# Optimization experiments

Hardware: AMD Instinct MI355X
Metric: run time of the kernel (lower is better)

Reference implementation:

```python
import jax, jax.numpy as jnp
import numpy as np

B, T = 64, 20          # batch, caption length
C, HW = 512, 196       # cnn_channels, width*height (14x14)
V, E, U = 10000, 256, 512  # n_tokens, emb_size, lstm_units
MAX_NORM = 5.0


def setup_inputs() -> dict:
    key = jax.random.key(0)
    ks = jax.random.split(key, 12)
    s = 0.02
    return {
        "image_features": jax.random.normal(ks[0], (B, C, HW), jnp.float32),
        "captions_ix": jax.random.randint(ks[1], (B, T), 0, V, dtype=jnp.int32),
        "W_h0": jax.random.normal(ks[2], (U, C), jnp.float32) * s,
        "b_h0": jnp.zeros((U,), jnp.float32),
        "W_c0": jax.random.normal(ks[3], (U, C), jnp.float32) * s,
        "b_c0": jnp.zeros((U,), jnp.float32),
        "emb": jax.random.normal(ks[4], (V, E), jnp.float32) * s,
        "W_key": jax.random.normal(ks[5], (U, C), jnp.float32) * s,
        "b_key": jnp.zeros((U,), jnp.float32),
        "W_ih": jax.random.normal(ks[6], (4 * U, C + E), jnp.float32) * s,
        "b_ih": jnp.zeros((4 * U,), jnp.float32),
        "W_hh": jax.random.normal(ks[7], (4 * U, U), jnp.float32) * s,
        "b_hh": jnp.zeros((4 * U,), jnp.float32),
        "W_out": jax.random.normal(ks[8], (V, C + E + U), jnp.float32) * s,
        "b_out": jnp.zeros((V,), jnp.float32),
    }


def _caption_net(image_features, captions_ix, W_h0, b_h0, W_c0, b_c0, emb,
                 W_key, b_key, W_ih, b_ih, W_hh, b_hh, W_out, b_out):
    feats_mean = image_features.mean(axis=2)                # [B, C]
    hid0 = feats_mean @ W_h0.T + b_h0                       # [B, U]
    cell0 = feats_mean @ W_c0.T + b_c0                      # [B, U]
    feats = jnp.transpose(image_features, (0, 2, 1))        # [B, HW, C]
    keys = feats @ W_key.T + b_key                          # [B, HW, U]

    # nn.Embedding(max_norm=5): renorm rows whose L2 norm exceeds 5
    norms = jnp.linalg.norm(emb, axis=1, keepdims=True)
    emb_eff = emb * jnp.minimum(1.0, MAX_NORM / jnp.maximum(norms, 1e-12))
    cap_emb = emb_eff[captions_ix]                          # [B, T, E]

    inv_scale = 1.0 / (keys.shape[2] ** 0.5)

    def step(carry, emb_t):
        hid, cell = carry
        # scaled dot-product attention, query = current hidden state
        scores = jnp.einsum('bu,bku->bk', hid, keys) * inv_scale   # [B, HW]
        w = jax.nn.softmax(scores, axis=1)
        a = jnp.einsum('bk,bkc->bc', w, feats)                     # [B, C]
        x = jnp.concatenate([emb_t, a], axis=1)                    # [B, E+C]
        gates = x @ W_ih.T + b_ih + hid @ W_hh.T + b_hh            # [B, 4U]
        i, f, g, o = jnp.split(gates, 4, axis=1)
        cell = jax.nn.sigmoid(f) * cell + jax.nn.sigmoid(i) * jnp.tanh(g)
        hid = jax.nn.sigmoid(o) * jnp.tanh(cell)
        out = jnp.concatenate([hid, a, emb_t], axis=1)             # [B, U+C+E]
        return (hid, cell), (out, w)

    (_, _), (outs, attn) = jax.lax.scan(step, (hid0, cell0),
                                        jnp.transpose(cap_emb, (1, 0, 2)))
    outs = jnp.transpose(outs, (1, 0, 2))                   # [B, T, U+C+E]
    attn = jnp.transpose(attn, (1, 0, 2))                   # [B, T, HW]
    logits = outs @ W_out.T + b_out                         # [B, T, V]
    return logits, attn


def reference(image_features, captions_ix, W_h0, b_h0, W_c0, b_c0, emb,
              W_key, b_key, W_ih, b_ih, W_hh, b_hh, W_out, b_out):
    return _caption_net(image_features, captions_ix, W_h0, b_h0, W_c0, b_c0,
                        emb, W_key, b_key, W_ih, b_ih, W_hh, b_hh, W_out, b_out)
```

## Files before the change

kernel.cpp:

```cpp
#include <hip/hip_runtime.h>
#include <math.h>

#define B 64
#define T 20
#define C 512
#define HW 196
#define V 10000
#define E 256
#define U 512
#define G4U 2048
#define ODIM 1280
#define KTOT 1280
#define NBLK 64

typedef short bf8_t __attribute__((ext_vector_type(8)));
typedef float f4_t  __attribute__((ext_vector_type(4)));
typedef _Float16 h2_t __attribute__((ext_vector_type(2)));

__device__ __forceinline__ unsigned short f2bf(float f) {
    unsigned int u = __float_as_uint(f);
    return (unsigned short)((u + 0x7fffu + ((u >> 16) & 1u)) >> 16);
}
__device__ __forceinline__ float bf2f(unsigned short s) {
    return __uint_as_float((unsigned int)s << 16);
}
__device__ __forceinline__ float bflo(unsigned int kv) { return __uint_as_float(kv << 16); }
__device__ __forceinline__ float bfhi(unsigned int kv) { return __uint_as_float(kv & 0xffff0000u); }
__device__ __forceinline__ unsigned short f2h(float f) {
    _Float16 h = (_Float16)f;
    return *(unsigned short*)&h;
}

__device__ __forceinline__ void coh_load4w(const void* p, uint4& r) {
    asm volatile("global_load_dwordx4 %0, %1, off sc0 sc1\n\t"
                 "s_waitcnt vmcnt(0)"
                 : "=&v"(r) : "v"(p) : "memory");
}
__device__ __forceinline__ void coh_load4_issue(const void* p, uint4& r) {
    asm volatile("global_load_dwordx4 %0, %1, off sc0 sc1"
                 : "=&v"(r) : "v"(p) : "memory");
}
__device__ __forceinline__ void wait_vm0() {
    asm volatile("s_waitcnt vmcnt(0)" ::: "memory");
    __builtin_amdgcn_sched_barrier(0);
}
__device__ __forceinline__ void coh_store1f(void* p, float v) {
    asm volatile("global_store_dword %0, %1, off sc0 sc1" :: "v"(p), "v"(v) : "memory");
}
__device__ __forceinline__ void coh_store1u(void* p, unsigned int v) {
    asm volatile("global_store_dword %0, %1, off sc0 sc1" :: "v"(p), "v"(v) : "memory");
}
__device__ __forceinline__ void coh_store_us(void* p, unsigned int v) {
    asm volatile("global_store_short %0, %1, off sc0 sc1" :: "v"(p), "v"(v) : "memory");
}
__device__ __forceinline__ int coh_load_int(const int* p) {
    int v;
    asm volatile("global_load_dword %0, %1, off sc0 sc1\n\t"
                 "s_waitcnt vmcnt(0)"
                 : "=v"(v) : "v"(p) : "memory");
    return v;
}
__device__ __forceinline__ void coh_store_int(int* p, int v) {
    asm volatile("global_store_dword %0, %1, off sc0 sc1" :: "v"(p), "v"(v) : "memory");
}

__device__ __forceinline__ void gbarf(int* barf, int e) {
    asm volatile("s_waitcnt vmcnt(0)" ::: "memory");
    __syncthreads();
    int tid = threadIdx.x;
    if (blockIdx.x == 0) {
        if (tid == 0) coh_store_int(barf + 16, e);
        if (tid < 64) {
            while (!__all(coh_load_int(barf + 16 + tid * 16) >= e)) {}
            if (tid == 0) coh_store_int(barf, e);
        }
    } else {
        if (tid == 0) {
            coh_store_int(barf + 16 + blockIdx.x * 16, e);
            while (coh_load_int(barf) < e) {}
        }
    }
    __syncthreads();
}

__global__ void k_mean(const float* __restrict__ img, float* __restrict__ fm) {
    int wave = threadIdx.x >> 6;
    int lane = threadIdx.x & 63;
    int row = blockIdx.x * 4 + wave;
    const float* p = img + (size_t)row * HW;
    float s = p[lane] + p[lane + 64] + p[lane + 128];
    if (lane < 4) s += p[lane + 192];
    for (int off = 32; off > 0; off >>= 1) s += __shfl_down(s, off, 64);
    if (lane == 0) fm[row] = s * (1.0f / HW);
}

__global__ void k_init(const float* __restrict__ fm,
                       const float* __restrict__ W_h0, const float* __restrict__ b_h0,
                       const float* __restrict__ W_c0, const float* __restrict__ b_c0,
                       unsigned short* __restrict__ xb, float* __restrict__ cell) {
    int wv = blockIdx.x * 4 + (threadIdx.x >> 6);
    int lane = threadIdx.x & 63;
    int which = wv >> 15;
    int r = wv & 32767;
    int b = r >> 9, u = r & 511;
    const float* W = which ? W_c0 : W_h0;
    const float* bias = which ? b_c0 : b_h0;
    const float* f = fm + b * C;
    const float* w = W + (size_t)u * C;
    float s = 0.f;
    #pragma unroll
    for (int c = 0; c < C; c += 64) s += f[c + lane] * w[c + lane];
    for (int off = 32; off > 0; off >>= 1) s += __shfl_down(s, off, 64);
    if (lane == 0) {
        float v = s + bias[u];
        if (which) cell[r] = v;
        else       xb[(size_t)b * KTOT + 768 + u] = f2bf(v);
    }
}

__global__ void k_wkt(const float* __restrict__ Wk, float* __restrict__ WkT) {
    __shared__ float tile[64][65];
    int u0 = blockIdx.x * 64, c0 = blockIdx.y * 64;
    int x = threadIdx.x & 63, y0 = threadIdx.x >> 6;
    #pragma unroll
    for (int i = 0; i < 16; i++) {
        int r = y0 * 16 + i;
        tile[r][x] = Wk[(size_t)(u0 + r) * C + c0 + x];
    }
    __syncthreads();
    #pragma unroll
    for (int i = 0; i < 16; i++) {
        int r = y0 * 16 + i;
        WkT[(size_t)(c0 + r) * U + u0 + x] = tile[x][r];
    }
}

__global__ __launch_bounds__(256) void k_keys(const float* __restrict__ img,
        const float* __restrict__ WkT, const float* __restrict__ b_key,
        unsigned short* __restrict__ keys2) {
    __shared__ unsigned short st[32][200];
    int b = blockIdx.x >> 4;
    int u0 = (blockIdx.x & 15) * 32;
    int wave = __builtin_amdgcn_readfirstlane(threadIdx.x >> 6);
    int lane = threadIdx.x & 63;
    int lk = lane < 49 ? lane : 48;
    const f4_t* imgb = (const f4_t*)(img + (size_t)b * C * HW);
    f4_t acc[8];
    #pragma unroll
    for (int j = 0; j < 8; j++) acc[j] = (f4_t){0.f, 0.f, 0.f, 0.f};
    const float* wp = WkT + u0 + wave * 8;
    for (int c = 0; c < C; c++) {
        f4_t v = imgb[c * 49 + lk];
        const float* w = wp + (size_t)c * U;
        #pragma unroll
        for (int j = 0; j < 8; j++) acc[j] += v * w[j];
    }
    if (lane < 49) {
        #pragma unroll
        for (int j = 0; j < 8; j++) {
            float bk = b_key[u0 + wave * 8 + j];
            int ul = wave * 8 + j;
            int k = lane * 4;
            st[ul][k + 0] = f2bf(acc[j].x + bk);
            st[ul][k + 1] = f2bf(acc[j].y + bk);
            st[ul][k + 2] = f2bf(acc[j].z + bk);
            st[ul][k + 3] = f2bf(acc[j].w + bk);
        }
    }
    __syncthreads();
    int ui = threadIdx.x & 15;
    int kr = threadIdx.x >> 4;
    #pragma unroll
    for (int pass = 0; pass < 13; pass++) {
        int k = pass * 16 + kr;
        if (k < HW) {
            unsigned int lo = st[ui * 2][k];
            unsigned int hi = st[ui * 2 + 1][k];
            *(unsigned int*)&keys2[((size_t)b * HW + k) * U + u0 + ui * 2] = (hi << 16) | lo;
        }
    }
}

__global__ void k_wg(const float* __restrict__ W_ih, const float* __restrict__ W_hh,
                     unsigned short* __restrict__ Wg) {
    int j = blockIdx.x;
    int tid = threadIdx.x;
    const float* s1 = W_ih + (size_t)j * 768;
    const float* s2 = W_hh + (size_t)j * 512;
    unsigned short* dst = Wg + (size_t)j * KTOT;
    #pragma unroll
    for (int p = 0; p < 3; p++) dst[tid + p * 256] = f2bf(s1[tid + p * 256]);
    #pragma unroll
    for (int p = 0; p < 2; p++) dst[768 + tid + p * 256] = f2bf(s2[tid + p * 256]);
}

__global__ void k_emb(const int* __restrict__ ix, const float* __restrict__ emb,
                      unsigned short* __restrict__ outs, int* __restrict__ barf) {
    int bt = blockIdx.x;
    int e = threadIdx.x;
    if (bt == 0) {
        for (int i = e; i < 1040; i += 256) barf[i] = 0;
    }
    int row = ix[bt];
    float v = emb[(size_t)row * E + e];
    __shared__ float red[4];
    float sq = v * v;
    for (int off = 32; off > 0; off >>= 1) sq += __shfl_down(sq, off, 64);
    int wave = e >> 6, lane = e & 63;
    if (lane == 0) red[wave] = sq;
    __syncthreads();
    float norm = sqrtf(red[0] + red[1] + red[2] + red[3]);
    float scale = fminf(1.0f, 5.0f / fmaxf(norm, 1e-12f));
    outs[(size_t)bt * ODIM + (U + C) + e] = f2bf(v * scale);
}

__global__ __launch_bounds__(256) void k_img(const float* __restrict__ img,
                                             unsigned short* __restrict__ img2) {
    int oid = blockIdx.x * 256 + threadIdx.x;
    int row = oid / 25, p = oid - row * 25;
    const float* src = img + (size_t)row * HW;
    unsigned short h[8];
    #pragma unroll
    for (int i = 0; i < 8; i++) {
        int k = p * 8 + i;
        float f = (k < HW) ? src[k] : 0.f;
        h[i] = f2h(f);
    }
    *(uint4*)&img2[(size_t)row * 200 + p * 8] = *(const uint4*)h;
}

__global__ __launch_bounds__(256) void k_wo(const float* __restrict__ W,
                                            unsigned short* __restrict__ Wb) {
    size_t i = ((size_t)blockIdx.x * 256 + threadIdx.x) * 8;
    float4 f0 = *(const float4*)(W + i);
    float4 f1 = *(const float4*)(W + i + 4);
    uint4 q;
    q.x = ((unsigned int)f2bf(f0.y) << 16) | f2bf(f0.x);
    q.y = ((unsigned int)f2bf(f0.w) << 16) | f2bf(f0.z);
    q.z = ((unsigned int)f2bf(f1.y) << 16) | f2bf(f1.x);
    q.w = ((unsigned int)f2bf(f1.w) << 16) | f2bf(f1.z);
    *(uint4*)(Wb + i) = q;
}

__global__ __launch_bounds__(512) void k_loop(
    unsigned short* __restrict__ outs, unsigned short* __restrict__ xb,
    const float* __restrict__ cell0, float* __restrict__ gates4,
    const unsigned short* __restrict__ keys2, const float* __restrict__ img,
    const unsigned short* __restrict__ img2,
    const float* __restrict__ b_ih, const float* __restrict__ b_hh,
    const unsigned short* __restrict__ Wg, float* __restrict__ attn,
    int* __restrict__ barf) {
    int b = blockIdx.x;
    int tid = threadIdx.x;
    int wave = __builtin_amdgcn_readfirstlane(tid >> 6);
    int lane = tid & 63;
    int m16 = lane & 15, quad = lane >> 4;
    __shared__ float hidS[U];
    __shared__ float wS[200];
    __shared__ float red[8];
    __shared__ __align__(16) unsigned int wH[100];
    __shared__ unsigned short As[64 * 320];

    float c_r = cell0[(size_t)b * U + tid];
    float bsum[4];
    #pragma unroll
    for (int q = 0; q < 4; q++)
        bsum[q] = b_ih[q * 512 + tid] + b_hh[q * 512 + tid];

    int j0g = b * 32;
    int mt = wave >> 1, nt = wave & 1;
    int arow = mt * 16 + m16;
    int srow = tid >> 3, sc8 = tid & 7;
    int ep = 0;

    for (int t = 0; t <= T; ++t) {
        if (t > 0) {
            uint4 r0;
            coh_load4w(gates4 + ((size_t)b * 512 + tid) * 4, r0);
            float4 gv = *(float4*)&r0;
            float g0f = gv.x + bsum[0];
            float g1f = gv.y + bsum[1];
            float g2f = gv.z + bsum[2];
            float g3f = gv.w + bsum[3];
            float si = 1.f / (1.f + expf(-g0f));
            float sf = 1.f / (1.f + expf(-g1f));
            float tg = tanhf(g2f);
            float so = 1.f / (1.f + expf(-g3f));
            float cn = sf * c_r + si * tg;
            c_r = cn;
            float hn = so * tanhf(cn);
            hidS[tid] = hn;
            unsigned int hv = f2bf(hn);
            outs[((size_t)b * T + (t - 1)) * ODIM + tid] = (unsigned short)hv;
            coh_store_us(&xb[(size_t)b * KTOT + 768 + tid], hv);
        } else {
            hidS[tid] = bf2f(xb[(size_t)b * KTOT + 768 + tid]);
        }
        if (t == T) break;
        __syncthreads();

        float sc = 0.f;
        if (tid < HW) {
            const uint4* kr = (const uint4*)(keys2 + ((size_t)b * HW + tid) * U);
            float acc = 0.f;
            #pragma unroll 8
            for (int i = 0; i < 64; i++) {
                uint4 kv = kr[i];
                float4 h0 = *(const float4*)&hidS[i * 8];
                float4 h1 = *(const float4*)&hidS[i * 8 + 4];
                acc += bflo(kv.x) * h0.x + bfhi(kv.x) * h0.y
                     + bflo(kv.y) * h0.z + bfhi(kv.y) * h0.w
                     + bflo(kv.z) * h1.x + bfhi(kv.z) * h1.y
                     + bflo(kv.w) * h1.z + bfhi(kv.w) * h1.w;
            }
            sc = acc * 0.044194173824159216f;
        }
        {
            float v = (tid < HW) ? sc : -1e30f;
            float m = v;
            for (int off = 32; off > 0; off >>= 1) m = fmaxf(m, __shfl_down(m, off, 64));
            if (lane == 0) red[wave] = m;
            __syncthreads();
            m = red[0];
            #pragma unroll
            for (int i = 1; i < 8; i++) m = fmaxf(m, red[i]);
            float ex = (tid < HW) ? expf(v - m) : 0.f;
            float ssum = ex;
            for (int off = 32; off > 0; off >>= 1) ssum += __shfl_down(ssum, off, 64);
            __syncthreads();
            if (lane == 0) red[wave] = ssum;
            __syncthreads();
            ssum = red[0];
            #pragma unroll
            for (int i = 1; i < 8; i++) ssum += red[i];
            float w = ex / ssum;
            if (tid < HW) {
                wS[tid] = w;
                attn[((size_t)b * T + t) * HW + tid] = w;
            } else if (tid < 200) {
                wS[tid] = 0.f;
            }
        }
        __syncthreads();
        if (tid < 100) {
            unsigned int lo = f2h(wS[2 * tid]);
            unsigned int hi = f2h(wS[2 * tid + 1]);
            wH[tid] = (hi << 16) | lo;
        }
        __syncthreads();

        {
            float acc = 0.f;
            if (img2) {
                const uint4* rowp = (const uint4*)(img2 + ((size_t)b * 512 + tid) * 200);
                const uint4* w4 = (const uint4*)wH;
                #pragma unroll
                for (int p = 0; p < 25; p++) {
                    uint4 v = rowp[p];
                    uint4 wv = w4[p];
                    const h2_t* va = (const h2_t*)&v;
                    const h2_t* wa = (const h2_t*)&wv;
#if __has_builtin(__builtin_amdgcn_fdot2)
                    acc = __builtin_amdgcn_fdot2(va[0], wa[0], acc, false);
                    acc = __builtin_amdgcn_fdot2(va[1], wa[1], acc, false);
                    acc = __builtin_amdgcn_fdot2(va[2], wa[2], acc, false);
                    acc = __builtin_amdgcn_fdot2(va[3], wa[3], acc, false);
#else
                    #pragma unroll
                    for (int q = 0; q < 4; q++) {
                        acc += (float)va[q][0] * (float)wa[q][0];
                        acc += (float)va[q][1] * (float)wa[q][1];
                    }
#endif
                }
            } else {
                const float4* rr4 = (const float4*)(img + (size_t)b * C * HW) + tid * 49;
                for (int k4 = 0; k4 < 49; k4++) {
                    float4 vv = rr4[k4];
                    acc += wS[4 * k4] * vv.x + wS[4 * k4 + 1] * vv.y
                         + wS[4 * k4 + 2] * vv.z + wS[4 * k4 + 3] * vv.w;
                }
            }
            unsigned int av = f2bf(acc);
            coh_store_us(&xb[(size_t)b * KTOT + 256 + tid], av);
            outs[((size_t)b * T + t) * ODIM + U + tid] = (unsigned short)av;
        }
        if (tid < 128) {
            const unsigned int* src = (const unsigned int*)(outs + ((size_t)b * T + t) * ODIM);
            unsigned int* dst = (unsigned int*)(xb + (size_t)b * KTOT);
            coh_store1u(&dst[tid], src[512 + tid]);
        }

        ++ep; gbarf(barf, ep);

        {
            f4_t acc2 = (f4_t){0.f, 0.f, 0.f, 0.f};
            #pragma unroll 1
            for (int s = 0; s < 4; s++) {
                int kbase = s * 320;
                uint4 ra[5];
                #pragma unroll
                for (int p = 0; p < 5; p++) {
                    int chunk = sc8 + 8 * p;
                    coh_load4_issue(&xb[(size_t)srow * KTOT + kbase + chunk * 8], ra[p]);
                }
                wait_vm0();
                #pragma unroll
                for (int p = 0; p < 5; p++) {
                    int chunk = sc8 + 8 * p;
                    *(uint4*)&As[srow * 320 + ((chunk * 8) ^ ((srow & 7) << 3))] = ra[p];
                }
                __syncthreads();
                #pragma unroll
                for (int c = 0; c < 10; c++) {
                    int kl = c * 32 + quad * 8;
                    bf8_t afr = *(const bf8_t*)&As[arow * 320 + (kl ^ ((arow & 7) << 3))];
                    int kg = kbase + kl;
                    bf8_t bfr = *(const bf8_t*)&Wg[(size_t)(j0g + nt * 16 + m16) * KTOT + kg];
                    acc2 = __builtin_amdgcn_mfma_f32_16x16x32_bf16(afr, bfr, acc2, 0, 0, 0);
                }
                __syncthreads();
            }
            int n = j0g + nt * 16 + m16;
            int qq = n >> 9, uu = n & 511;
            #pragma unroll
            for (int rr = 0; rr < 4; rr++) {
                int bb = mt * 16 + quad * 4 + rr;
                coh_store1f(&gates4[((size_t)bb * 512 + uu) * 4 + qq], acc2[rr]);
            }
        }

        ++ep; gbarf(barf, ep);
    }
}

__global__ __launch_bounds__(256) void k_logits4(
    const unsigned short* __restrict__ A, const float* __restrict__ Wo,
    const float* __restrict__ bo, float* __restrict__ Cout) {
    __shared__ unsigned short As[128][72];
    __shared__ unsigned short Bs[128][72];
    int n0 = blockIdx.x * 128;
    int m0 = blockIdx.y * 128;
    int tid = threadIdx.x;
    int lane = tid & 63, wv = tid >> 6;
    int mw = (wv >> 1) * 64, nw = (wv & 1) * 64;
    int m16 = lane & 15, quad = lane >> 4;
    int srow = tid >> 1, shalf = tid & 1;

    f4_t acc[4][4];
    #pragma unroll
    for (int i = 0; i < 4; i++)
        #pragma unroll
        for (int j = 0; j < 4; j++)
            acc[i][j] = (f4_t){0.f, 0.f, 0.f, 0.f};

    for (int k0 = 0; k0 < KTOT; k0 += 64) {
        {
            const uint4* ap = (const uint4*)&A[(size_t)(m0 + srow) * KTOT + k0 + shalf * 32];
            uint4 a0 = ap[0], a1 = ap[1], a2 = ap[2], a3 = ap[3];
            uint4* dst = (uint4*)&As[srow][shalf * 32];
            dst[0] = a0; dst[1] = a1; dst[2] = a2; dst[3] = a3;
        }
        {
            int n = n0 + srow;
            uint4 q[4];
            if (n < V) {
                const float4* bp = (const float4*)&Wo[(size_t)n * KTOT + k0 + shalf * 32];
                #pragma unroll
                for (int g = 0; g < 4; g++) {
                    float4 f0 = bp[g * 2], f1 = bp[g * 2 + 1];
                    q[g].x = ((unsigned int)f2bf(f0.y) << 16) | f2bf(f0.x);
                    q[g].y = ((unsigned int)f2bf(f0.w) << 16) | f2bf(f0.z);
                    q[g].z = ((unsigned int)f2bf(f1.y) << 16) | f2bf(f1.x);
                    q[g].w = ((unsigned int)f2bf(f1.w) << 16) | f2bf(f1.z);
                }
            } else {
                #pragma unroll
                for (int g = 0; g < 4; g++) q[g] = (uint4){0u, 0u, 0u, 0u};
            }
            uint4* dst = (uint4*)&Bs[srow][shalf * 32];
            #pragma unroll
            for (int g = 0; g < 4; g++) dst[g] = q[g];
        }
        __syncthreads();
        #pragma unroll
        for (int h = 0; h < 2; h++) {
            bf8_t af[4], bf[4];
            #pragma unroll
            for (int i = 0; i < 4; i++)
                af[i] = *(const bf8_t*)&As[mw + i * 16 + m16][h * 32 + quad * 8];
            #pragma unroll
            for (int j = 0; j < 4; j++)
                bf[j] = *(const bf8_t*)&Bs[nw + j * 16 + m16][h * 32 + quad * 8];
            #pragma unroll
            for (int i = 0; i < 4; i++)
                #pragma unroll
                for (int j = 0; j < 4; j++)
                    acc[i][j] = __builtin_amdgcn_mfma_f32_16x16x32_bf16(af[i], bf[j], acc[i][j], 0, 0, 0);
        }
        __syncthreads();
    }

    #pragma unroll
    for (int j = 0; j < 4; j++) {
        int n = n0 + nw + j * 16 + m16;
        if (n >= V) continue;
        float bias = bo[n];
        #pragma unroll
        for (int i = 0; i < 4; i++) {
            int mb = m0 + mw + i * 16 + quad * 4;
            #pragma unroll
            for (int r = 0; r < 4; r++)
                Cout[(size_t)(mb + r) * V + n] = acc[i][j][r] + bias;
        }
    }
}

__global__ __launch_bounds__(256) void k_logits5(
    const unsigned short* __restrict__ A, const unsigned short* __restrict__ Wob,
    const float* __restrict__ bo, float* __restrict__ Cout) {
    __shared__ unsigned short As[128][72];
    __shared__ unsigned short Bs[128][72];
    int n0 = blockIdx.x * 128;
    int m0 = blockIdx.y * 128;
    int tid = threadIdx.x;
    int lane = tid & 63, wv = tid >> 6;
    int mw = (wv >> 1) * 64, nw = (wv & 1) * 64;
    int m16 = lane & 15, quad = lane >> 4;
    int srow = tid >> 1, shalf = tid & 1;

    f4_t acc[4][4];
    #pragma unroll
    for (int i = 0; i < 4; i++)
        #pragma unroll
        for (int j = 0; j < 4; j++)
            acc[i][j] = (f4_t){0.f, 0.f, 0.f, 0.f};

    for (int k0 = 0; k0 < KTOT; k0 += 64) {
        {
            const uint4* ap = (const uint4*)&A[(size_t)(m0 + srow) * KTOT + k0 + shalf * 32];
            uint4 a0 = ap[0], a1 = ap[1], a2 = ap[2], a3 = ap[3];
            uint4* dst = (uint4*)&As[srow][shalf * 32];
            dst[0] = a0; dst[1] = a1; dst[2] = a2; dst[3] = a3;
        }
        {
            int n = n0 + srow;
            uint4 q[4];
            if (n < V) {
                const uint4* bp = (const uint4*)&Wob[(size_t)n * KTOT + k0 + shalf * 32];
                #pragma unroll
                for (int g = 0; g < 4; g++) q[g] = bp[g];
            } else {
                #pragma unroll
                for (int g = 0; g < 4; g++) q[g] = (uint4){0u, 0u, 0u, 0u};
            }
            uint4* dst = (uint4*)&Bs[srow][shalf * 32];
            #pragma unroll
            for (int g = 0; g < 4; g++) dst[g] = q[g];
        }
        __syncthreads();
        #pragma unroll
        for (int h = 0; h < 2; h++) {
            bf8_t af[4], bf[4];
            #pragma unroll
            for (int i = 0; i < 4; i++)
                af[i] = *(const bf8_t*)&As[mw + i * 16 + m16][h * 32 + quad * 8];
            #pragma unroll
            for (int j = 0; j < 4; j++)
                bf[j] = *(const bf8_t*)&Bs[nw + j * 16 + m16][h * 32 + quad * 8];
            #pragma unroll
            for (int i = 0; i < 4; i++)
                #pragma unroll
                for (int j = 0; j < 4; j++)
                    acc[i][j] = __builtin_amdgcn_mfma_f32_16x16x32_bf16(af[i], bf[j], acc[i][j], 0, 0, 0);
        }
        __syncthreads();
    }

    #pragma unroll
    for (int j = 0; j < 4; j++) {
        int n = n0 + nw + j * 16 + m16;
        if (n >= V) continue;
        float bias = bo[n];
        #pragma unroll
        for (int i = 0; i < 4; i++) {
            int mb = m0 + mw + i * 16 + quad * 4;
            #pragma unroll
            for (int r = 0; r < 4; r++)
                Cout[(size_t)(mb + r) * V + n] = acc[i][j][r] + bias;
        }
    }
}

extern "C" void kernel_launch(void* const* d_in, const int* in_sizes, int n_in,
                              void* d_out, int out_size, void* d_ws, size_t ws_size,
                              hipStream_t stream) {
    const float* img   = (const float*)d_in[0];
    const int*   capix = (const int*)d_in[1];
    const float* W_h0  = (const float*)d_in[2];
    const float* b_h0  = (const float*)d_in[3];
    const float* W_c0  = (const float*)d_in[4];
    const float* b_c0  = (const float*)d_in[5];
    const float* emb   = (const float*)d_in[6];
    const float* W_key = (const float*)d_in[7];
    const float* b_key = (const float*)d_in[8];
    const float* W_ih  = (const float*)d_in[9];
    const float* b_ih  = (const float*)d_in[10];
    const float* W_hh  = (const float*)d_in[11];
    const float* b_hh  = (const float*)d_in[12];
    const float* W_out = (const float*)d_in[13];
    const float* b_out = (const float*)d_in[14];

    float* ws = (float*)d_ws;
    float* gates4    = ws;
    float* fm        = ws;
    float* cell      = gates4 + 131072;
    float* WkT       = cell + 32768;
    int*   barf      = (int*)WkT;
    unsigned short* Wg    = (unsigned short*)(WkT + 262144);
    unsigned short* xb    = Wg + 2621440;
    unsigned short* outs  = xb + 81920;
    unsigned short* keys2 = outs + (size_t)B * T * ODIM;
    const size_t IMG2_OFF = 23232576;
    unsigned short* img2 = (unsigned short*)((char*)d_ws + IMG2_OFF);
    bool use_img2 = ws_size >= IMG2_OFF + (size_t)B * C * 200 * 2;
    const size_t WOB_OFF = 36339776;
    unsigned short* Wob = (unsigned short*)((char*)d_ws + WOB_OFF);
    bool use_wob = ws_size >= WOB_OFF + (size_t)V * KTOT * 2;

    float* logits = (float*)d_out;
    float* attn   = logits + (size_t)B * T * V;

    k_mean<<<(B * C) / 4, 256, 0, stream>>>(img, fm);
    k_init<<<(2 * B * U) / 4, 256, 0, stream>>>(fm, W_h0, b_h0, W_c0, b_c0, xb, cell);
    k_wkt<<<dim3(8, 8), 256, 0, stream>>>(W_key, WkT);
    k_keys<<<B * 16, 256, 0, stream>>>(img, WkT, b_key, keys2);
    k_wg<<<G4U, 256, 0, stream>>>(W_ih, W_hh, Wg);
    k_emb<<<B * T, 256, 0, stream>>>(capix, emb, outs, barf);
    if (use_img2)
        k_img<<<3200, 256, 0, stream>>>(img, img2);
    if (use_wob)
        k_wo<<<(V * KTOT) / 2048, 256, 0, stream>>>(W_out, Wob);

    k_loop<<<NBLK, 512, 0, stream>>>(outs, xb, cell, gates4, keys2, img,
                                     use_img2 ? img2 : (const unsigned short*)nullptr,
                                     b_ih, b_hh, Wg, attn, barf);

    if (use_wob)
        k_logits5<<<dim3((V + 127) / 128, (B * T) / 128), 256, 0, stream>>>(outs, Wob, b_out, logits);
    else
        k_logits4<<<dim3((V + 127) / 128, (B * T) / 128), 256, 0, stream>>>(outs, W_out, b_out, logits);
}
```

Baseline: 1.179 ms.

## Stage step inputs in LDS, vectorize coherent stores, and prefetch gate GEMM tiles

The per-step x vector (embedding, attention context, hidden state) is now assembled in shared memory and written to global memory with 16-byte coherent stores, replacing many 2- and 4-byte scattered stores. Gate outputs are transposed through an LDS tile so each thread issues one dwordx4 store in a contiguous [b][4U] layout, and the reader switches to four scalar coherent loads. The K-chunk loads for the gate MFMA loop are double-buffered so the next chunk is fetched while the current one is computed. The barrier spin loops also gain s_sleep to reduce polling pressure, at the risk of adding wake-up latency to every grid barrier.

```diff
diff --git a/kernel.cpp b/kernel.cpp
--- a/kernel.cpp
+++ b/kernel.cpp
@@ -15,6 +15,7 @@
 
 typedef short bf8_t __attribute__((ext_vector_type(8)));
 typedef float f4_t  __attribute__((ext_vector_type(4)));
+typedef unsigned int u32x4 __attribute__((ext_vector_type(4)));
 typedef _Float16 h2_t __attribute__((ext_vector_type(2)));
 
 __device__ __forceinline__ unsigned short f2bf(float f) {
@@ -31,11 +32,6 @@
     return *(unsigned short*)&h;
 }
 
-__device__ __forceinline__ void coh_load4w(const void* p, uint4& r) {
-    asm volatile("global_load_dwordx4 %0, %1, off sc0 sc1\n\t"
-                 "s_waitcnt vmcnt(0)"
-                 : "=&v"(r) : "v"(p) : "memory");
-}
 __device__ __forceinline__ void coh_load4_issue(const void* p, uint4& r) {
     asm volatile("global_load_dwordx4 %0, %1, off sc0 sc1"
                  : "=&v"(r) : "v"(p) : "memory");
@@ -44,14 +40,22 @@
     asm volatile("s_waitcnt vmcnt(0)" ::: "memory");
     __builtin_amdgcn_sched_barrier(0);
 }
-__device__ __forceinline__ void coh_store1f(void* p, float v) {
-    asm volatile("global_store_dword %0, %1, off sc0 sc1" :: "v"(p), "v"(v) : "memory");
-}
-__device__ __forceinline__ void coh_store1u(void* p, unsigned int v) {
-    asm volatile("global_store_dword %0, %1, off sc0 sc1" :: "v"(p), "v"(v) : "memory");
-}
-__device__ __forceinline__ void coh_store_us(void* p, unsigned int v) {
-    asm volatile("global_store_short %0, %1, off sc0 sc1" :: "v"(p), "v"(v) : "memory");
+__device__ __forceinline__ void coh_load1x4(const void* p0, const void* p1,
+                                            const void* p2, const void* p3,
+                                            float& r0, float& r1, float& r2, float& r3) {
+    asm volatile("global_load_dword %0, %4, off sc0 sc1\n\t"
+                 "global_load_dword %1, %5, off sc0 sc1\n\t"
+                 "global_load_dword %2, %6, off sc0 sc1\n\t"
+                 "global_load_dword %3, %7, off sc0 sc1\n\t"
+                 "s_waitcnt vmcnt(0)"
+                 : "=&v"(r0), "=&v"(r1), "=&v"(r2), "=&v"(r3)
+                 : "v"(p0), "v"(p1), "v"(p2), "v"(p3) : "memory");
+}
+__device__ __forceinline__ void coh_store4u(void* p, u32x4 v) {
+    asm volatile("global_store_dwordx4 %0, %1, off sc0 sc1" :: "v"(p), "v"(v) : "memory");
+}
+__device__ __forceinline__ void coh_store4f(void* p, f4_t v) {
+    asm volatile("global_store_dwordx4 %0, %1, off sc0 sc1" :: "v"(p), "v"(v) : "memory");
 }
 __device__ __forceinline__ int coh_load_int(const int* p) {
     int v;
@@ -71,13 +75,15 @@
     if (blockIdx.x == 0) {
         if (tid == 0) coh_store_int(barf + 16, e);
         if (tid < 64) {
-            while (!__all(coh_load_int(barf + 16 + tid * 16) >= e)) {}
+            while (!__all(coh_load_int(barf + 16 + tid * 16) >= e))
+                __builtin_amdgcn_s_sleep(1);
             if (tid == 0) coh_store_int(barf, e);
         }
     } else {
         if (tid == 0) {
             coh_store_int(barf + 16 + blockIdx.x * 16, e);
-            while (coh_load_int(barf) < e) {}
+            while (coh_load_int(barf) < e)
+                __builtin_amdgcn_s_sleep(2);
         }
     }
     __syncthreads();
@@ -259,6 +265,8 @@
     __shared__ float wS[200];
     __shared__ float red[8];
     __shared__ __align__(16) unsigned int wH[100];
+    __shared__ __align__(16) unsigned short xbS[KTOT];
+    __shared__ __align__(16) float gS[64][36];
     __shared__ unsigned short As[64 * 320];
 
     float c_r = cell0[(size_t)b * U + tid];
@@ -275,13 +283,13 @@
 
     for (int t = 0; t <= T; ++t) {
         if (t > 0) {
-            uint4 r0;
-            coh_load4w(gates4 + ((size_t)b * 512 + tid) * 4, r0);
-            float4 gv = *(float4*)&r0;
-            float g0f = gv.x + bsum[0];
-            float g1f = gv.y + bsum[1];
-            float g2f = gv.z + bsum[2];
-            float g3f = gv.w + bsum[3];
+            const float* gb = gates4 + (size_t)b * 2048 + tid;
+            float ga0, ga1, ga2, ga3;
+            coh_load1x4(gb, gb + 512, gb + 1024, gb + 1536, ga0, ga1, ga2, ga3);
+            float g0f = ga0 + bsum[0];
+            float g1f = ga1 + bsum[1];
+            float g2f = ga2 + bsum[2];
+            float g3f = ga3 + bsum[3];
             float si = 1.f / (1.f + expf(-g0f));
             float sf = 1.f / (1.f + expf(-g1f));
             float tg = tanhf(g2f);
@@ -292,9 +300,11 @@
             hidS[tid] = hn;
             unsigned int hv = f2bf(hn);
             outs[((size_t)b * T + (t - 1)) * ODIM + tid] = (unsigned short)hv;
-            coh_store_us(&xb[(size_t)b * KTOT + 768 + tid], hv);
+            xbS[768 + tid] = (unsigned short)hv;
         } else {
-            hidS[tid] = bf2f(xb[(size_t)b * KTOT + 768 + tid]);
+            unsigned short hs = xb[(size_t)b * KTOT + 768 + tid];
+            hidS[tid] = bf2f(hs);
+            xbS[768 + tid] = hs;
         }
         if (t == T) break;
         __syncthreads();
@@ -382,35 +392,42 @@
                 }
             }
             unsigned int av = f2bf(acc);
-            coh_store_us(&xb[(size_t)b * KTOT + 256 + tid], av);
+            xbS[256 + tid] = (unsigned short)av;
             outs[((size_t)b * T + t) * ODIM + U + tid] = (unsigned short)av;
         }
         if (tid < 128) {
             const unsigned int* src = (const unsigned int*)(outs + ((size_t)b * T + t) * ODIM);
-            unsigned int* dst = (unsigned int*)(xb + (size_t)b * KTOT);
-            coh_store1u(&dst[tid], src[512 + tid]);
-        }
+            ((unsigned int*)xbS)[tid] = src[512 + tid];
+        }
+        __syncthreads();
+        if (tid < 160)
+            coh_store4u(&xb[(size_t)b * KTOT + tid * 8], ((const u32x4*)xbS)[tid]);
 
         ++ep; gbarf(barf, ep);
 
         {
             f4_t acc2 = (f4_t){0.f, 0.f, 0.f, 0.f};
+            const unsigned short* xrow = xb + (size_t)srow * KTOT;
+            uint4 ra[5];
+            #pragma unroll
+            for (int p = 0; p < 5; p++)
+                coh_load4_issue(xrow + (sc8 + 8 * p) * 8, ra[p]);
+            wait_vm0();
             #pragma unroll 1
             for (int s = 0; s < 4; s++) {
-                int kbase = s * 320;
-                uint4 ra[5];
-                #pragma unroll
-                for (int p = 0; p < 5; p++) {
-                    int chunk = sc8 + 8 * p;
-                    coh_load4_issue(&xb[(size_t)srow * KTOT + kbase + chunk * 8], ra[p]);
-                }
-                wait_vm0();
                 #pragma unroll
                 for (int p = 0; p < 5; p++) {
                     int chunk = sc8 + 8 * p;
                     *(uint4*)&As[srow * 320 + ((chunk * 8) ^ ((srow & 7) << 3))] = ra[p];
                 }
                 __syncthreads();
+                if (s < 3) {
+                    int kb2 = (s + 1) * 320;
+                    #pragma unroll
+                    for (int p = 0; p < 5; p++)
+                        coh_load4_issue(xrow + kb2 + (sc8 + 8 * p) * 8, ra[p]);
+                }
+                int kbase = s * 320;
                 #pragma unroll
                 for (int c = 0; c < 10; c++) {
                     int kl = c * 32 + quad * 8;
@@ -419,14 +436,17 @@
                     bf8_t bfr = *(const bf8_t*)&Wg[(size_t)(j0g + nt * 16 + m16) * KTOT + kg];
                     acc2 = __builtin_amdgcn_mfma_f32_16x16x32_bf16(afr, bfr, acc2, 0, 0, 0);
                 }
+                if (s < 3) wait_vm0();
                 __syncthreads();
             }
-            int n = j0g + nt * 16 + m16;
-            int qq = n >> 9, uu = n & 511;
-            #pragma unroll
-            for (int rr = 0; rr < 4; rr++) {
-                int bb = mt * 16 + quad * 4 + rr;
-                coh_store1f(&gates4[((size_t)bb * 512 + uu) * 4 + qq], acc2[rr]);
+            #pragma unroll
+            for (int rr = 0; rr < 4; rr++)
+                gS[mt * 16 + quad * 4 + rr][nt * 16 + m16] = acc2[rr];
+            __syncthreads();
+            {
+                int row = tid >> 3, c4 = tid & 7;
+                f4_t v = *(const f4_t*)&gS[row][c4 * 4];
+                coh_store4f(&gates4[(size_t)row * 2048 + j0g + c4 * 4], v);
             }
         }
 
```

After: 1.196 ms. About the same (+1.4%).

## Replace grid-barrier MFMA gate GEMM with per-batch-block fp16 dot-product GEMV

Applied to the files above, without the earlier changes.

The recurrent loop no longer splits the gate GEMM across blocks with two software grid barriers per timestep. Each block now owns one batch row and computes all 2048 gate outputs itself, using fp16 fdot2 against a transposed, k4-interleaved fp16 copy of the combined W_ih/W_hh weights. This removes the global barrier spin-waits and the coherent global traffic for gates and xb. In exchange every block streams the full 5 MB weight matrix each step, about 100 MB per step across 64 blocks, and drops MFMA for scalar dot products. Gate inputs also move from bf16 to fp16 precision.

```diff
diff --git a/kernel.cpp b/kernel.cpp
--- a/kernel.cpp
+++ b/kernel.cpp
@@ -8,7 +8,6 @@
 #define V 10000
 #define E 256
 #define U 512
-#define G4U 2048
 #define ODIM 1280
 #define KTOT 1280
 #define NBLK 64
@@ -29,58 +28,6 @@
 __device__ __forceinline__ unsigned short f2h(float f) {
     _Float16 h = (_Float16)f;
     return *(unsigned short*)&h;
-}
-
-__device__ __forceinline__ void coh_load4w(const void* p, uint4& r) {
-    asm volatile("global_load_dwordx4 %0, %1, off sc0 sc1\n\t"
-                 "s_waitcnt vmcnt(0)"
-                 : "=&v"(r) : "v"(p) : "memory");
-}
-__device__ __forceinline__ void coh_load4_issue(const void* p, uint4& r) {
-    asm volatile("global_load_dwordx4 %0, %1, off sc0 sc1"
-                 : "=&v"(r) : "v"(p) : "memory");
-}
-__device__ __forceinline__ void wait_vm0() {
-    asm volatile("s_waitcnt vmcnt(0)" ::: "memory");
-    __builtin_amdgcn_sched_barrier(0);
-}
-__device__ __forceinline__ void coh_store1f(void* p, float v) {
-    asm volatile("global_store_dword %0, %1, off sc0 sc1" :: "v"(p), "v"(v) : "memory");
-}
-__device__ __forceinline__ void coh_store1u(void* p, unsigned int v) {
-    asm volatile("global_store_dword %0, %1, off sc0 sc1" :: "v"(p), "v"(v) : "memory");
-}
-__device__ __forceinline__ void coh_store_us(void* p, unsigned int v) {
-    asm volatile("global_store_short %0, %1, off sc0 sc1" :: "v"(p), "v"(v) : "memory");
-}
-__device__ __forceinline__ int coh_load_int(const int* p) {
-    int v;
-    asm volatile("global_load_dword %0, %1, off sc0 sc1\n\t"
-                 "s_waitcnt vmcnt(0)"
-                 : "=v"(v) : "v"(p) : "memory");
-    return v;
-}
-__device__ __forceinline__ void coh_store_int(int* p, int v) {
-    asm volatile("global_store_dword %0, %1, off sc0 sc1" :: "v"(p), "v"(v) : "memory");
-}
-
-__device__ __forceinline__ void gbarf(int* barf, int e) {
-    asm volatile("s_waitcnt vmcnt(0)" ::: "memory");
-    __syncthreads();
-    int tid = threadIdx.x;
-    if (blockIdx.x == 0) {
-        if (tid == 0) coh_store_int(barf + 16, e);
-        if (tid < 64) {
-            while (!__all(coh_load_int(barf + 16 + tid * 16) >= e)) {}
-            if (tid == 0) coh_store_int(barf, e);
-        }
-    } else {
-        if (tid == 0) {
-            coh_store_int(barf + 16 + blockIdx.x * 16, e);
-            while (coh_load_int(barf) < e) {}
-        }
-    }
-    __syncthreads();
 }
 
 __global__ void k_mean(const float* __restrict__ img, float* __restrict__ fm) {
@@ -97,7 +44,7 @@
 __global__ void k_init(const float* __restrict__ fm,
                        const float* __restrict__ W_h0, const float* __restrict__ b_h0,
                        const float* __restrict__ W_c0, const float* __restrict__ b_c0,
-                       unsigned short* __restrict__ xb, float* __restrict__ cell) {
+                       unsigned short* __restrict__ hid0b, float* __restrict__ cell) {
     int wv = blockIdx.x * 4 + (threadIdx.x >> 6);
     int lane = threadIdx.x & 63;
     int which = wv >> 15;
@@ -114,7 +61,7 @@
     if (lane == 0) {
         float v = s + bias[u];
         if (which) cell[r] = v;
-        else       xb[(size_t)b * KTOT + 768 + u] = f2bf(v);
+        else       hid0b[(size_t)b * U + u] = f2bf(v);
     }
 }
 
@@ -181,26 +128,29 @@
     }
 }
 
-__global__ void k_wg(const float* __restrict__ W_ih, const float* __restrict__ W_hh,
-                     unsigned short* __restrict__ Wg) {
-    int j = blockIdx.x;
-    int tid = threadIdx.x;
-    const float* s1 = W_ih + (size_t)j * 768;
-    const float* s2 = W_hh + (size_t)j * 512;
-    unsigned short* dst = Wg + (size_t)j * KTOT;
-    #pragma unroll
-    for (int p = 0; p < 3; p++) dst[tid + p * 256] = f2bf(s1[tid + p * 256]);
-    #pragma unroll
-    for (int p = 0; p < 2; p++) dst[768 + tid + p * 256] = f2bf(s2[tid + p * 256]);
+__global__ __launch_bounds__(256) void k_wgT(const float* __restrict__ W_ih,
+                                             const float* __restrict__ W_hh,
+                                             unsigned short* __restrict__ WgT4) {
+    int k4 = blockIdx.x;
+    int j = blockIdx.y * 256 + threadIdx.x;
+    float f0, f1, f2, f3;
+    if (k4 < 192) {
+        const float* s = W_ih + (size_t)j * 768 + k4 * 4;
+        f0 = s[0]; f1 = s[1]; f2 = s[2]; f3 = s[3];
+    } else {
+        const float* s = W_hh + (size_t)j * 512 + (k4 - 192) * 4;
+        f0 = s[0]; f1 = s[1]; f2 = s[2]; f3 = s[3];
+    }
+    uint2 v;
+    v.x = ((unsigned int)f2h(f1) << 16) | f2h(f0);
+    v.y = ((unsigned int)f2h(f3) << 16) | f2h(f2);
+    ((uint2*)WgT4)[(size_t)k4 * 2048 + j] = v;
 }
 
 __global__ void k_emb(const int* __restrict__ ix, const float* __restrict__ emb,
-                      unsigned short* __restrict__ outs, int* __restrict__ barf) {
+                      unsigned short* __restrict__ outs) {
     int bt = blockIdx.x;
     int e = threadIdx.x;
-    if (bt == 0) {
-        for (int i = e; i < 1040; i += 256) barf[i] = 0;
-    }
     int row = ix[bt];
     float v = emb[(size_t)row * E + e];
     __shared__ float red[4];
@@ -242,24 +192,23 @@
     *(uint4*)(Wb + i) = q;
 }
 
-__global__ __launch_bounds__(512) void k_loop(
-    unsigned short* __restrict__ outs, unsigned short* __restrict__ xb,
-    const float* __restrict__ cell0, float* __restrict__ gates4,
+__global__ __launch_bounds__(512) void k_loop2(
+    unsigned short* __restrict__ outs, const unsigned short* __restrict__ hid0b,
+    const float* __restrict__ cell0,
     const unsigned short* __restrict__ keys2, const float* __restrict__ img,
     const unsigned short* __restrict__ img2,
+    const unsigned short* __restrict__ WgT4,
     const float* __restrict__ b_ih, const float* __restrict__ b_hh,
-    const unsigned short* __restrict__ Wg, float* __restrict__ attn,
-    int* __restrict__ barf) {
+    float* __restrict__ attn) {
     int b = blockIdx.x;
     int tid = threadIdx.x;
     int wave = __builtin_amdgcn_readfirstlane(tid >> 6);
     int lane = tid & 63;
-    int m16 = lane & 15, quad = lane >> 4;
     __shared__ float hidS[U];
     __shared__ float wS[200];
     __shared__ float red[8];
     __shared__ __align__(16) unsigned int wH[100];
-    __shared__ unsigned short As[64 * 320];
+    __shared__ __align__(16) unsigned short xbH[KTOT];
 
     float c_r = cell0[(size_t)b * U + tid];
     float bsum[4];
@@ -267,38 +216,10 @@
     for (int q = 0; q < 4; q++)
         bsum[q] = b_ih[q * 512 + tid] + b_hh[q * 512 + tid];
 
-    int j0g = b * 32;
-    int mt = wave >> 1, nt = wave & 1;
-    int arow = mt * 16 + m16;
-    int srow = tid >> 3, sc8 = tid & 7;
-    int ep = 0;
-
-    for (int t = 0; t <= T; ++t) {
-        if (t > 0) {
-            uint4 r0;
-            coh_load4w(gates4 + ((size_t)b * 512 + tid) * 4, r0);
-            float4 gv = *(float4*)&r0;
-            float g0f = gv.x + bsum[0];
-            float g1f = gv.y + bsum[1];
-            float g2f = gv.z + bsum[2];
-            float g3f = gv.w + bsum[3];
-            float si = 1.f / (1.f + expf(-g0f));
-            float sf = 1.f / (1.f + expf(-g1f));
-            float tg = tanhf(g2f);
-            float so = 1.f / (1.f + expf(-g3f));
-            float cn = sf * c_r + si * tg;
-            c_r = cn;
-            float hn = so * tanhf(cn);
-            hidS[tid] = hn;
-            unsigned int hv = f2bf(hn);
-            outs[((size_t)b * T + (t - 1)) * ODIM + tid] = (unsigned short)hv;
-            coh_store_us(&xb[(size_t)b * KTOT + 768 + tid], hv);
-        } else {
-            hidS[tid] = bf2f(xb[(size_t)b * KTOT + 768 + tid]);
-        }
-        if (t == T) break;
-        __syncthreads();
-
+    hidS[tid] = bf2f(hid0b[(size_t)b * U + tid]);
+    __syncthreads();
+
+    for (int t = 0; t < T; ++t) {
         float sc = 0.f;
         if (tid < HW) {
             const uint4* kr = (const uint4*)(keys2 + ((size_t)b * HW + tid) * U);
@@ -381,56 +302,60 @@
                          + wS[4 * k4 + 2] * vv.z + wS[4 * k4 + 3] * vv.w;
                 }
             }
-            unsigned int av = f2bf(acc);
-            coh_store_us(&xb[(size_t)b * KTOT + 256 + tid], av);
-            outs[((size_t)b * T + t) * ODIM + U + tid] = (unsigned short)av;
+            xbH[256 + tid] = f2h(acc);
+            outs[((size_t)b * T + t) * ODIM + U + tid] = f2bf(acc);
+            xbH[768 + tid] = f2h(hidS[tid]);
         }
         if (tid < 128) {
-            const unsigned int* src = (const unsigned int*)(outs + ((size_t)b * T + t) * ODIM);
-            unsigned int* dst = (unsigned int*)(xb + (size_t)b * KTOT);
-            coh_store1u(&dst[tid], src[512 + tid]);
-        }
-
-        ++ep; gbarf(barf, ep);
-
-        {
-            f4_t acc2 = (f4_t){0.f, 0.f, 0.f, 0.f};
-            #pragma unroll 1
-            for (int s = 0; s < 4; s++) {
-                int kbase = s * 320;
-                uint4 ra[5];
-                #pragma unroll
-                for (int p = 0; p < 5; p++) {
-                    int chunk = sc8 + 8 * p;
-                    coh_load4_issue(&xb[(size_t)srow * KTOT + kbase + chunk * 8], ra[p]);
+            unsigned int us = ((const unsigned int*)(outs + ((size_t)b * T + t) * ODIM))[512 + tid];
+            unsigned int h0 = f2h(bf2f((unsigned short)(us & 0xffffu)));
+            unsigned int h1 = f2h(bf2f((unsigned short)(us >> 16)));
+            ((unsigned int*)xbH)[tid] = (h1 << 16) | h0;
+        }
+        __syncthreads();
+
+        f4_t acc4 = (f4_t){0.f, 0.f, 0.f, 0.f};
+        {
+            const uint2* Wp = (const uint2*)WgT4;
+            const uint2* xp = (const uint2*)xbH;
+            #pragma unroll 4
+            for (int k4 = 0; k4 < 320; k4++) {
+                uint2 xq = xp[k4];
+                const h2_t* xa = (const h2_t*)&xq;
+                const uint2* wrow = Wp + (size_t)k4 * 2048 + tid;
+                #pragma unroll
+                for (int q = 0; q < 4; q++) {
+                    uint2 wv = wrow[q * 512];
+                    const h2_t* wa = (const h2_t*)&wv;
+#if __has_builtin(__builtin_amdgcn_fdot2)
+                    acc4[q] = __builtin_amdgcn_fdot2(wa[0], xa[0], acc4[q], false);
+                    acc4[q] = __builtin_amdgcn_fdot2(wa[1], xa[1], acc4[q], false);
+#else
+                    acc4[q] += (float)wa[0][0] * (float)xa[0][0];
+                    acc4[q] += (float)wa[0][1] * (float)xa[0][1];
+                    acc4[q] += (float)wa[1][0] * (float)xa[1][0];
+                    acc4[q] += (float)wa[1][1] * (float)xa[1][1];
+#endif
                 }
-                wait_vm0();
-                #pragma unroll
-                for (int p = 0; p < 5; p++) {
-                    int chunk = sc8 + 8 * p;
-                    *(uint4*)&As[srow * 320 + ((chunk * 8) ^ ((srow & 7) << 3))] = ra[p];
-                }
-                __syncthreads();
-                #pragma unroll
-                for (int c = 0; c < 10; c++) {
-                    int kl = c * 32 + quad * 8;
-                    bf8_t afr = *(const bf8_t*)&As[arow * 320 + (kl ^ ((arow & 7) << 3))];
-                    int kg = kbase + kl;
-                    bf8_t bfr = *(const bf8_t*)&Wg[(size_t)(j0g + nt * 16 + m16) * KTOT + kg];
-                    acc2 = __builtin_amdgcn_mfma_f32_16x16x32_bf16(afr, bfr, acc2, 0, 0, 0);
-                }
-                __syncthreads();
             }
-            int n = j0g + nt * 16 + m16;
-            int qq = n >> 9, uu = n & 511;
-            #pragma unroll
-            for (int rr = 0; rr < 4; rr++) {
-                int bb = mt * 16 + quad * 4 + rr;
-                coh_store1f(&gates4[((size_t)bb * 512 + uu) * 4 + qq], acc2[rr]);
-            }
-        }
-
-        ++ep; gbarf(barf, ep);
+        }
+
+        {
+            float g0f = acc4[0] + bsum[0];
+            float g1f = acc4[1] + bsum[1];
+            float g2f = acc4[2] + bsum[2];
+            float g3f = acc4[3] + bsum[3];
+            float si = 1.f / (1.f + expf(-g0f));
+            float sf = 1.f / (1.f + expf(-g1f));
+            float tg = tanhf(g2f);
+            float so = 1.f / (1.f + expf(-g3f));
+            float cn = sf * c_r + si * tg;
+            c_r = cn;
+            float hn = so * tanhf(cn);
+            outs[((size_t)b * T + t) * ODIM + tid] = f2bf(hn);
+            hidS[tid] = hn;
+        }
+        __syncthreads();
     }
 }
 
@@ -612,14 +537,13 @@
     const float* b_out = (const float*)d_in[14];
 
     float* ws = (float*)d_ws;
-    float* gates4    = ws;
+    float* scratch   = ws;
     float* fm        = ws;
-    float* cell      = gates4 + 131072;
+    float* cell      = scratch + 131072;
     float* WkT       = cell + 32768;
-    int*   barf      = (int*)WkT;
-    unsigned short* Wg    = (unsigned short*)(WkT + 262144);
-    unsigned short* xb    = Wg + 2621440;
-    unsigned short* outs  = xb + 81920;
+    unsigned short* WgT4  = (unsigned short*)(WkT + 262144);
+    unsigned short* hid0b = WgT4 + 2621440;
+    unsigned short* outs  = hid0b + 81920;
     unsigned short* keys2 = outs + (size_t)B * T * ODIM;
     const size_t IMG2_OFF = 23232576;
     unsigned short* img2 = (unsigned short*)((char*)d_ws + IMG2_OFF);
@@ -632,19 +556,19 @@
     float* attn   = logits + (size_t)B * T * V;
 
     k_mean<<<(B * C) / 4, 256, 0, stream>>>(img, fm);
-    k_init<<<(2 * B * U) / 4, 256, 0, stream>>>(fm, W_h0, b_h0, W_c0, b_c0, xb, cell);
+    k_init<<<(2 * B * U) / 4, 256, 0, stream>>>(fm, W_h0, b_h0, W_c0, b_c0, hid0b, cell);
     k_wkt<<<dim3(8, 8), 256, 0, stream>>>(W_key, WkT);
     k_keys<<<B * 16, 256, 0, stream>>>(img, WkT, b_key, keys2);
-    k_wg<<<G4U, 256, 0, stream>>>(W_ih, W_hh, Wg);
-    k_emb<<<B * T, 256, 0, stream>>>(capix, emb, outs, barf);
+    k_wgT<<<dim3(320, 8), 256, 0, stream>>>(W_ih, W_hh, WgT4);
+    k_emb<<<B * T, 256, 0, stream>>>(capix, emb, outs);
     if (use_img2)
         k_img<<<3200, 256, 0, stream>>>(img, img2);
     if (use_wob)
         k_wo<<<(V * KTOT) / 2048, 256, 0, stream>>>(W_out, Wob);
 
-    k_loop<<<NBLK, 512, 0, stream>>>(outs, xb, cell, gates4, keys2, img,
-                                     use_img2 ? img2 : (const unsigned short*)nullptr,
-                                     b_ih, b_hh, Wg, attn, barf);
+    k_loop2<<<NBLK, 512, 0, stream>>>(outs, hid0b, cell, keys2, img,
+                                      use_img2 ? img2 : (const unsigned short*)nullptr,
+                                      WgT4, b_ih, b_hh, attn);
 
     if (use_wob)
         k_logits5<<<dim3((V + 127) / 128, (B * T) / 128), 256, 0, stream>>>(outs, Wob, b_out, logits);
```

Result: slower. 2.201 ms (+86.6%).
